# Optimization experiments

Hardware: AMD Instinct MI355X
Metric: run time of the kernel (lower is better)

The kernel has to match this reference:

```python
import jax, jax.numpy as jnp
import numpy as np

IN_DIM = 256
QK_DIM = IN_DIM // 8


def setup_inputs() -> dict:
    key = jax.random.key(0)
    ks = jax.random.split(key, 10)
    B, C, W, H = 4, IN_DIM, 64, 64
    a = jax.random.normal(ks[0], (B, C, W, H), dtype=jnp.float32)
    b = jax.random.normal(ks[1], (B, C, W, H), dtype=jnp.float32)
    c = jax.random.uniform(ks[2], (B, 1, 2 * W, 2 * H), dtype=jnp.float32)
    scale = 0.02
    wq = jax.random.normal(ks[3], (QK_DIM, C), dtype=jnp.float32) * scale
    bq = jnp.zeros((QK_DIM,), dtype=jnp.float32)
    wk = jax.random.normal(ks[4], (QK_DIM, C), dtype=jnp.float32) * scale
    bk = jnp.zeros((QK_DIM,), dtype=jnp.float32)
    wv = jax.random.normal(ks[5], (C, C), dtype=jnp.float32) * scale
    bv = jnp.zeros((C,), dtype=jnp.float32)
    gamma = jnp.ones((1,), dtype=jnp.float32)
    return {"a": a, "b": b, "c": c, "wq": wq, "bq": bq, "wk": wk,
            "bk": bk, "wv": wv, "bv": bv, "gamma": gamma}


def reference(a, b, c, wq, bq, wk, bk, wv, bv, gamma):
    B, C, W, H = a.shape
    N = W * H
    # F.interpolate(c, scale_factor=1/down_rate, mode='nearest'): output idx i -> input idx i*down_rate
    down = c.shape[2] // W
    cd = c[:, :, ::down, ::down]                      # [B,1,W,H]
    # 1x1 convs as channel contractions
    q = jnp.einsum('bchw,oc->bohw', a, wq) + bq[None, :, None, None]
    k = jnp.einsum('bchw,oc->bohw', b, wk) + bk[None, :, None, None]
    v = jnp.einsum('bchw,oc->bohw', a, wv) + bv[None, :, None, None]
    qf = q.reshape(B, QK_DIM, N)                      # proj_query^T rows are spatial
    kf = k.reshape(B, QK_DIM, N)
    vf = v.reshape(B, C, N)
    sim = jnp.einsum('bdi,bdj->bij', qf, kf)          # [B,N,N]
    cflat = cd.reshape(B, N)
    # mask[b,i,j] = cflat[b,i] (per-query multiplicative logit scaling)
    logits = sim * cflat[:, :, None]
    attn = jax.nn.softmax(logits, axis=-1)            # [B,N,N]
    out_attn = jnp.einsum('bcj,bij->bci', vf, attn).reshape(B, C, W, H)
    out = gamma * a * cd + (1.0 - cd) * out_attn
    return out
```

## Files before the change

### kernel.cpp

```cpp
#include <hip/hip_runtime.h>

#define LOG2E 1.44269504088896340736f

typedef __attribute__((ext_vector_type(8))) short short8;
typedef __attribute__((ext_vector_type(4))) float float4v;
typedef __attribute__((ext_vector_type(2))) float float2v;
typedef __attribute__((ext_vector_type(2))) int int2v;
typedef __attribute__((ext_vector_type(4))) int int4v;

__device__ inline unsigned short f2bf(float f) {
    union { float f; unsigned u; } v; v.f = f;
    unsigned r = v.u + 0x7fffu + ((v.u >> 16) & 1u);
    return (unsigned short)(r >> 16);
}
__device__ inline float bf2f(unsigned short u) {
    union { unsigned u; float f; } v; v.u = ((unsigned)u) << 16;
    return v.f;
}
__device__ inline unsigned pk_bf16(float a, float b) {
    union { float f; unsigned u; } ua, ub; ua.f = a; ub.f = b;
    return __builtin_amdgcn_perm(ub.u + 0x8000u, ua.u + 0x8000u, 0x07060302u);
}
__device__ inline unsigned cvtpk_bf16(float a, float b) {
    unsigned r;
    asm("v_cvt_pk_bf16_f32 %0, %1, %2" : "=v"(r) : "v"(a), "v"(b));
    return r;
}

__global__ void wcvt_kernel(const float* __restrict__ wq, const float* __restrict__ wk,
                            const float* __restrict__ wv, unsigned short* __restrict__ Wbf)
{
    int idx = blockIdx.x * 256 + threadIdx.x;
    int e4  = idx * 4;
    int row = e4 >> 8, col = e4 & 255;
    const float* src = (row < 32) ? (wq + row * 256 + col)
                     : (row < 64) ? (wk + (row - 32) * 256 + col)
                                  : (wv + (row - 64) * 256 + col);
    float4v v = *(const float4v*)src;
    int2v p;
    p.x = (unsigned)f2bf(v[0]) | ((unsigned)f2bf(v[1]) << 16);
    p.y = (unsigned)f2bf(v[2]) | ((unsigned)f2bf(v[3]) << 16);
    *(int2v*)(Wbf + e4) = p;
}

__launch_bounds__(512, 4)
__global__ void proj_kernel(const float* __restrict__ a_p, const float* __restrict__ b_p,
                            const float* __restrict__ c_p,
                            const float* __restrict__ bq, const float* __restrict__ bk,
                            const float* __restrict__ bv,
                            const unsigned short* __restrict__ Wbf,
                            unsigned short* __restrict__ Qg, unsigned short* __restrict__ Kg,
                            unsigned short* __restrict__ Vg)
{
    __shared__ __align__(16) unsigned short At[32 * 266];
    __shared__ __align__(16) unsigned short Bt[32 * 266];
    __shared__ float bias[320];
    __shared__ float cdl[32];

    const int t    = threadIdx.x;
    const int blk  = blockIdx.x;
    const int b    = blk & 3;
    const int tile = blk >> 2;
    const int i0   = tile * 32;
    const int lane = t & 63;
    const int w    = t >> 6;
    const int q    = lane >> 4;
    const int n    = lane & 15;
    const int it   = w & 1;
    const int mh   = w >> 1;

    {
        const int arr = t >> 8, tt = t & 255;
        unsigned* dst = (unsigned*)(arr ? Bt : At);
        const float* base = (arr ? b_p : a_p) + (size_t)b * 256 * 4096 + i0;
#pragma unroll
        for (int r = 0; r < 4; ++r) {
            int task = r * 256 + tt;
            int cp = task >> 3, px4 = (task & 7) * 4;
            const float* s0 = base + (size_t)(2 * cp) * 4096 + px4;
            float4v r0 = *(const float4v*)s0;
            float4v r1 = *(const float4v*)(s0 + 4096);
#pragma unroll
            for (int k = 0; k < 4; ++k)
                dst[(px4 + k) * 133 + cp] = pk_bf16(r0[k], r1[k]);
        }
        if (t < 320) bias[t] = (t < 32) ? bq[t] : (t < 64) ? bk[t - 32] : bv[t - 64];
        else if (t < 352) {
            int u = t - 320;
            cdl[u] = c_p[b * 16384 + (tile >> 1) * 256 + (tile & 1) * 64 + u * 2];
        }
    }
    __syncthreads();

    float4v acc[5];
#pragma unroll
    for (int j = 0; j < 5; ++j) acc[j] = (float4v){0.f, 0.f, 0.f, 0.f};

#pragma unroll 2
    for (int kc = 0; kc < 8; ++kc) {
        short8 xa = *(const short8*)&At[(it * 16 + n) * 266 + kc * 32 + q * 8];
        short8 xb = xa;
        if (mh == 0)
            xb = *(const short8*)&Bt[(it * 16 + n) * 266 + kc * 32 + q * 8];
#pragma unroll
        for (int j = 0; j < 5; ++j) {
            int mt = mh * 5 + j;
            short8 wf = *(const short8*)(Wbf + (size_t)(mt * 16 + n) * 256 + kc * 32 + q * 8);
            short8 bsel = (mt == 2 || mt == 3) ? xb : xa;
            acc[j] = __builtin_amdgcn_mfma_f32_16x16x32_bf16(wf, bsel, acc[j], 0, 0, 0);
        }
    }
    __syncthreads();

    unsigned short* QKst = At;
    unsigned short* Vst  = Bt;
    {
        const float cdq = cdl[it * 16 + n] * LOG2E;
#pragma unroll
        for (int j = 0; j < 5; ++j) {
            int mt = mh * 5 + j;
            float4v bv4 = *(const float4v*)&bias[mt * 16 + q * 4];
            float v0 = acc[j][0] + bv4[0], v1 = acc[j][1] + bv4[1];
            float v2 = acc[j][2] + bv4[2], v3 = acc[j][3] + bv4[3];
            if (mt < 2) {
                v0 *= cdq; v1 *= cdq; v2 *= cdq; v3 *= cdq;
                int2v pk; pk.x = (int)pk_bf16(v0, v1); pk.y = (int)pk_bf16(v2, v3);
                *(int2v*)&QKst[(it * 16 + n) * 72 + mt * 16 + q * 4] = pk;
            } else if (mt < 4) {
                int2v pk; pk.x = (int)pk_bf16(v0, v1); pk.y = (int)pk_bf16(v2, v3);
                *(int2v*)&QKst[(it * 16 + n) * 72 + mt * 16 + q * 4] = pk;
            } else {
                int p = ((n >> 2) * 8) + (it * 4) + (n & 3);
                int cbase = mt * 16 - 64 + q * 4;
                Vst[(cbase + 0) * 32 + p] = f2bf(v0);
                Vst[(cbase + 1) * 32 + p] = f2bf(v1);
                Vst[(cbase + 2) * 32 + p] = f2bf(v2);
                Vst[(cbase + 3) * 32 + p] = f2bf(v3);
            }
        }
    }
    __syncthreads();

    if (t < 256) {
        int i = t >> 3, h8 = t & 7;
        int4v v = *(const int4v*)&QKst[i * 72 + h8 * 8];
        unsigned short* dstp = (h8 < 4)
            ? Qg + (size_t)(b * 4096 + i0 + i) * 32 + h8 * 8
            : Kg + (size_t)(b * 4096 + i0 + i) * 32 + (h8 - 4) * 8;
        *(int4v*)dstp = v;
    }
    {
#pragma unroll
        for (int k = 0; k < 2; ++k) {
            int flat = k * 512 + t;
            int4v v = *(const int4v*)&Vst[flat * 8];
            *(int4v*)(Vg + (size_t)(b * 128 + tile) * 8192 + (size_t)flat * 8) = v;
        }
    }
}

__launch_bounds__(256, 3)
__global__ void attn_kernel(const unsigned short* __restrict__ Qg,
                            const unsigned short* __restrict__ Kg,
                            const unsigned short* __restrict__ Vg,
                            unsigned short* __restrict__ Opart, float* __restrict__ lsum)
{
    const int t    = threadIdx.x;
    const int blk  = blockIdx.x;
    const int b    = blk & 3;
    const int rt   = (blk >> 2) & 63;
    const int s    = blk >> 8;
    const int ni   = (s == 2) ? 32 : 48;
    const int lidx = (s << 8) | (rt << 2) | b;
    const int i0   = rt * 64;
    const int lane = t & 63;
    const int w    = t >> 6;
    const int q    = lane >> 4;
    const int n    = lane & 15;

    short8 qf[4];
#pragma unroll
    for (int ig = 0; ig < 4; ++ig)
        qf[ig] = *(const short8*)(Qg + (size_t)(b * 4096 + i0 + ig * 16 + n) * 32 + q * 8);

    float4v acc[4][4];
#pragma unroll
    for (int ig = 0; ig < 4; ++ig)
#pragma unroll
        for (int ct = 0; ct < 4; ++ct) acc[ig][ct] = (float4v){0.f, 0.f, 0.f, 0.f};
    float lsc[4] = {0.f, 0.f, 0.f, 0.f};

    const float4v m16v = (float4v){-16.f, -16.f, -16.f, -16.f};

    const unsigned short* kb = Kg + (size_t)(b * 4096 + s * 1536 + n) * 32 + q * 8;
    const unsigned short* vb = Vg + ((size_t)((b * 128 + s * 48) * 256 + w * 64 + n)) * 32 + q * 8;

    short8 vf[4];
#pragma unroll
    for (int ct = 0; ct < 4; ++ct)
        vf[ct] = *(const short8*)(vb + ct * 512);
    short8 kf0 = *(const short8*)(kb);
    short8 kf1 = *(const short8*)(kb + 512);

    short8 pfc[4];
    {
        float4v s0[4], s1[4];
#pragma unroll
        for (int ig = 0; ig < 4; ++ig) {
            s0[ig] = __builtin_amdgcn_mfma_f32_16x16x32_bf16(kf0, qf[ig], m16v, 0, 0, 0);
            s1[ig] = __builtin_amdgcn_mfma_f32_16x16x32_bf16(kf1, qf[ig], m16v, 0, 0, 0);
        }
        kf0 = *(const short8*)(kb + 1024);
        kf1 = *(const short8*)(kb + 1536);
#pragma unroll
        for (int ig = 0; ig < 4; ++ig) {
            float p0 = __builtin_amdgcn_exp2f(s0[ig][0]), p1 = __builtin_amdgcn_exp2f(s0[ig][1]);
            float p2 = __builtin_amdgcn_exp2f(s0[ig][2]), p3 = __builtin_amdgcn_exp2f(s0[ig][3]);
            float p4 = __builtin_amdgcn_exp2f(s1[ig][0]), p5 = __builtin_amdgcn_exp2f(s1[ig][1]);
            float p6 = __builtin_amdgcn_exp2f(s1[ig][2]), p7 = __builtin_amdgcn_exp2f(s1[ig][3]);
            lsc[ig] += ((p0 + p1) + (p2 + p3)) + ((p4 + p5) + (p6 + p7));
            union { short8 s8; unsigned u[4]; } pf_;
            pf_.u[0] = cvtpk_bf16(p0, p1);
            pf_.u[1] = cvtpk_bf16(p2, p3);
            pf_.u[2] = cvtpk_bf16(p4, p5);
            pf_.u[3] = cvtpk_bf16(p6, p7);
            pfc[ig] = pf_.s8;
        }
    }
    kb += 2048;
    vb += 8192;

#pragma unroll 1
    for (int it = 0; it < ni - 1; ++it) {
        float4v s0[4], s1[4];
#pragma unroll
        for (int ig = 0; ig < 4; ++ig) {
            s0[ig] = __builtin_amdgcn_mfma_f32_16x16x32_bf16(kf0, qf[ig], m16v, 0, 0, 0);
            s1[ig] = __builtin_amdgcn_mfma_f32_16x16x32_bf16(kf1, qf[ig], m16v, 0, 0, 0);
        }
        kf0 = *(const short8*)(kb);
        kf1 = *(const short8*)(kb + 512);

        __builtin_amdgcn_s_setprio(1);
#pragma unroll
        for (int ig = 0; ig < 4; ++ig)
#pragma unroll
            for (int ct = 0; ct < 4; ++ct)
                acc[ig][ct] = __builtin_amdgcn_mfma_f32_16x16x32_bf16(pfc[ig], vf[ct], acc[ig][ct], 0, 0, 0);
        __builtin_amdgcn_s_setprio(0);

#pragma unroll
        for (int ct = 0; ct < 4; ++ct)
            vf[ct] = *(const short8*)(vb + ct * 512);

#pragma unroll
        for (int ig = 0; ig < 4; ++ig) {
            float p0 = __builtin_amdgcn_exp2f(s0[ig][0]), p1 = __builtin_amdgcn_exp2f(s0[ig][1]);
            float p2 = __builtin_amdgcn_exp2f(s0[ig][2]), p3 = __builtin_amdgcn_exp2f(s0[ig][3]);
            float p4 = __builtin_amdgcn_exp2f(s1[ig][0]), p5 = __builtin_amdgcn_exp2f(s1[ig][1]);
            float p6 = __builtin_amdgcn_exp2f(s1[ig][2]), p7 = __builtin_amdgcn_exp2f(s1[ig][3]);
            lsc[ig] += ((p0 + p1) + (p2 + p3)) + ((p4 + p5) + (p6 + p7));
            union { short8 s8; unsigned u[4]; } pf_;
            pf_.u[0] = cvtpk_bf16(p0, p1);
            pf_.u[1] = cvtpk_bf16(p2, p3);
            pf_.u[2] = cvtpk_bf16(p4, p5);
            pf_.u[3] = cvtpk_bf16(p6, p7);
            pfc[ig] = pf_.s8;
        }

        kb += 1024;
        vb += 8192;
    }

#pragma unroll
    for (int ig = 0; ig < 4; ++ig)
#pragma unroll
        for (int ct = 0; ct < 4; ++ct)
            acc[ig][ct] = __builtin_amdgcn_mfma_f32_16x16x32_bf16(pfc[ig], vf[ct], acc[ig][ct], 0, 0, 0);

    const size_t obase = (size_t)lidx * 16384;
#pragma unroll
    for (int ig = 0; ig < 4; ++ig)
#pragma unroll
        for (int ct = 0; ct < 4; ++ct) {
            int c = w * 64 + ct * 16 + n;
            int i = ig * 16 + q * 4;
            int2v pk;
            pk.x = (int)pk_bf16(acc[ig][ct][0], acc[ig][ct][1]);
            pk.y = (int)pk_bf16(acc[ig][ct][2], acc[ig][ct][3]);
            *(int2v*)(Opart + obase + (size_t)c * 64 + i) = pk;
        }
#pragma unroll
    for (int ig = 0; ig < 4; ++ig) {
        float v = lsc[ig];
        v += __shfl_xor(v, 16, 64);
        v += __shfl_xor(v, 32, 64);
        if (w == 0 && lane < 16)
            lsum[(size_t)lidx * 64 + ig * 16 + lane] = v;
    }
}

__launch_bounds__(256, 4)
__global__ void combine_kernel(const float* __restrict__ a_p, const float* __restrict__ c_p,
                               const float* __restrict__ gamma_p,
                               const unsigned short* __restrict__ Opart,
                               const float* __restrict__ lsum, float* __restrict__ out)
{
    __shared__ float invL[64];
    __shared__ float cdl[64];

    const int t   = threadIdx.x;
    const int blk = blockIdx.x;
    const int b   = blk & 3;
    const int rt  = (blk >> 2) & 63;
    const int cs  = blk >> 8;
    const int i0  = rt * 64;

    if (t < 64) {
        float L = 0.f;
#pragma unroll
        for (int s = 0; s < 3; ++s)
            L += lsum[(size_t)((s << 8) | (rt << 2) | b) * 64 + t];
        invL[t] = 1.0f / L;
        cdl[t] = c_p[b * 16384 + rt * 256 + 2 * t];
    }
    __syncthreads();

    const float gam = gamma_p[0];
    const int c  = cs * 32 + (t >> 3);
    const int e8 = (t & 7) * 8;
    float o[8];
#pragma unroll
    for (int r = 0; r < 8; ++r) o[r] = 0.f;
#pragma unroll
    for (int s = 0; s < 3; ++s) {
        int idx = (s << 8) | (rt << 2) | b;
        int4v pv = *(const int4v*)(Opart + (size_t)idx * 16384 + (size_t)c * 64 + e8);
#pragma unroll
        for (int h = 0; h < 4; ++h) {
            unsigned u = (unsigned)pv[h];
            o[2 * h]     += bf2f((unsigned short)(u & 0xffffu));
            o[2 * h + 1] += bf2f((unsigned short)(u >> 16));
        }
    }
    size_t gi = (size_t)(b * 256 + c) * 4096 + i0 + e8;
    float4v a0 = *(const float4v*)(a_p + gi);
    float4v a1 = *(const float4v*)(a_p + gi + 4);
    float4v ov0, ov1;
#pragma unroll
    for (int r = 0; r < 4; ++r) {
        float cd0 = cdl[e8 + r],     l0 = invL[e8 + r];
        float cd1 = cdl[e8 + 4 + r], l1 = invL[e8 + 4 + r];
        ov0[r] = gam * a0[r] * cd0 + (1.0f - cd0) * (o[r] * l0);
        ov1[r] = gam * a1[r] * cd1 + (1.0f - cd1) * (o[4 + r] * l1);
    }
    *(float4v*)(out + gi) = ov0;
    *(float4v*)(out + gi + 4) = ov1;
}

extern "C" void kernel_launch(void* const* d_in, const int* in_sizes, int n_in,
                              void* d_out, int out_size, void* d_ws, size_t ws_size,
                              hipStream_t stream)
{
    const float* a_p   = (const float*)d_in[0];
    const float* b_p   = (const float*)d_in[1];
    const float* c_p   = (const float*)d_in[2];
    const float* wq    = (const float*)d_in[3];
    const float* bq    = (const float*)d_in[4];
    const float* wk    = (const float*)d_in[5];
    const float* bk    = (const float*)d_in[6];
    const float* wv    = (const float*)d_in[7];
    const float* bv    = (const float*)d_in[8];
    const float* gamma = (const float*)d_in[9];
    float* out = (float*)d_out;

    unsigned short* Qg    = (unsigned short*)d_ws;
    unsigned short* Kg    = Qg + (size_t)4 * 4096 * 32;
    unsigned short* Vg    = Kg + (size_t)4 * 4096 * 32;
    unsigned short* Wbf   = Vg + (size_t)4 * 256 * 4096;
    unsigned short* Opart = Wbf + (size_t)320 * 256;
    float*          lsum  = (float*)(Opart + (size_t)768 * 16384);

    wcvt_kernel<<<80, 256, 0, stream>>>(wq, wk, wv, Wbf);
    proj_kernel<<<512, 512, 0, stream>>>(a_p, b_p, c_p, bq, bk, bv, Wbf, Qg, Kg, Vg);
    attn_kernel<<<768, 256, 0, stream>>>(Qg, Kg, Vg, Opart, lsum);
    combine_kernel<<<2048, 256, 0, stream>>>(a_p, c_p, gamma, Opart, lsum, out);
}
```

Measured before the change: 180.6 us.

## Fuse weight bf16 conversion into projection kernel and double pixel tile

Removes the separate weight-conversion kernel launch. The projection kernel now reads fp32 weights directly and converts them to bf16 on the fly. Each block covers 64 pixels instead of 32, so it launches half as many blocks, and each wave computes 10 output tiles instead of 5. This saves a launch and the Wbf round trip, but every block converts weights redundantly, and the larger tile raises register and LDS use and lowers occupancy.

```diff
diff --git a/kernel.cpp b/kernel.cpp
--- a/kernel.cpp
+++ b/kernel.cpp
@@ -27,56 +27,41 @@
     return r;
 }
 
-__global__ void wcvt_kernel(const float* __restrict__ wq, const float* __restrict__ wk,
-                            const float* __restrict__ wv, unsigned short* __restrict__ Wbf)
-{
-    int idx = blockIdx.x * 256 + threadIdx.x;
-    int e4  = idx * 4;
-    int row = e4 >> 8, col = e4 & 255;
-    const float* src = (row < 32) ? (wq + row * 256 + col)
-                     : (row < 64) ? (wk + (row - 32) * 256 + col)
-                                  : (wv + (row - 64) * 256 + col);
-    float4v v = *(const float4v*)src;
-    int2v p;
-    p.x = (unsigned)f2bf(v[0]) | ((unsigned)f2bf(v[1]) << 16);
-    p.y = (unsigned)f2bf(v[2]) | ((unsigned)f2bf(v[3]) << 16);
-    *(int2v*)(Wbf + e4) = p;
-}
-
-__launch_bounds__(512, 4)
+__launch_bounds__(512, 2)
 __global__ void proj_kernel(const float* __restrict__ a_p, const float* __restrict__ b_p,
                             const float* __restrict__ c_p,
+                            const float* __restrict__ wq_p, const float* __restrict__ wk_p,
+                            const float* __restrict__ wv_p,
                             const float* __restrict__ bq, const float* __restrict__ bk,
                             const float* __restrict__ bv,
-                            const unsigned short* __restrict__ Wbf,
                             unsigned short* __restrict__ Qg, unsigned short* __restrict__ Kg,
                             unsigned short* __restrict__ Vg)
 {
-    __shared__ __align__(16) unsigned short At[32 * 266];
-    __shared__ __align__(16) unsigned short Bt[32 * 266];
+    __shared__ __align__(16) unsigned short At[64 * 266];
+    __shared__ __align__(16) unsigned short Bt[64 * 266];
     __shared__ float bias[320];
-    __shared__ float cdl[32];
+    __shared__ float cdl[64];
 
     const int t    = threadIdx.x;
     const int blk  = blockIdx.x;
     const int b    = blk & 3;
     const int tile = blk >> 2;
-    const int i0   = tile * 32;
+    const int i0   = tile * 64;
     const int lane = t & 63;
     const int w    = t >> 6;
     const int q    = lane >> 4;
     const int n    = lane & 15;
-    const int it   = w & 1;
-    const int mh   = w >> 1;
+    const int it   = w & 3;
+    const int mh   = w >> 2;
 
     {
         const int arr = t >> 8, tt = t & 255;
         unsigned* dst = (unsigned*)(arr ? Bt : At);
         const float* base = (arr ? b_p : a_p) + (size_t)b * 256 * 4096 + i0;
 #pragma unroll
-        for (int r = 0; r < 4; ++r) {
+        for (int r = 0; r < 8; ++r) {
             int task = r * 256 + tt;
-            int cp = task >> 3, px4 = (task & 7) * 4;
+            int cp = task >> 4, px4 = (task & 15) * 4;
             const float* s0 = base + (size_t)(2 * cp) * 4096 + px4;
             float4v r0 = *(const float4v*)s0;
             float4v r1 = *(const float4v*)(s0 + 4096);
@@ -85,16 +70,13 @@
                 dst[(px4 + k) * 133 + cp] = pk_bf16(r0[k], r1[k]);
         }
         if (t < 320) bias[t] = (t < 32) ? bq[t] : (t < 64) ? bk[t - 32] : bv[t - 64];
-        else if (t < 352) {
-            int u = t - 320;
-            cdl[u] = c_p[b * 16384 + (tile >> 1) * 256 + (tile & 1) * 64 + u * 2];
-        }
+        else if (t < 384) cdl[t - 320] = c_p[b * 16384 + tile * 256 + (t - 320) * 2];
     }
     __syncthreads();
 
-    float4v acc[5];
-#pragma unroll
-    for (int j = 0; j < 5; ++j) acc[j] = (float4v){0.f, 0.f, 0.f, 0.f};
+    float4v acc[10];
+#pragma unroll
+    for (int j = 0; j < 10; ++j) acc[j] = (float4v){0.f, 0.f, 0.f, 0.f};
 
 #pragma unroll 2
     for (int kc = 0; kc < 8; ++kc) {
@@ -103,11 +85,21 @@
         if (mh == 0)
             xb = *(const short8*)&Bt[(it * 16 + n) * 266 + kc * 32 + q * 8];
 #pragma unroll
-        for (int j = 0; j < 5; ++j) {
-            int mt = mh * 5 + j;
-            short8 wf = *(const short8*)(Wbf + (size_t)(mt * 16 + n) * 256 + kc * 32 + q * 8);
+        for (int j = 0; j < 10; ++j) {
+            int mt = mh * 10 + j;
+            const float* wbase = (mt < 2) ? wq_p : (mt < 4) ? wk_p : wv_p;
+            int mrow = (mt < 2) ? (mt * 16 + n) : (mt < 4) ? ((mt - 2) * 16 + n)
+                                                           : ((mt - 4) * 16 + n);
+            const float* wp = wbase + (size_t)mrow * 256 + kc * 32 + q * 8;
+            float4v wa = *(const float4v*)wp;
+            float4v wb2 = *(const float4v*)(wp + 4);
+            union { short8 s8; unsigned u[4]; } wf_;
+            wf_.u[0] = pk_bf16(wa[0], wa[1]);
+            wf_.u[1] = pk_bf16(wa[2], wa[3]);
+            wf_.u[2] = pk_bf16(wb2[0], wb2[1]);
+            wf_.u[3] = pk_bf16(wb2[2], wb2[3]);
             short8 bsel = (mt == 2 || mt == 3) ? xb : xa;
-            acc[j] = __builtin_amdgcn_mfma_f32_16x16x32_bf16(wf, bsel, acc[j], 0, 0, 0);
+            acc[j] = __builtin_amdgcn_mfma_f32_16x16x32_bf16(wf_.s8, bsel, acc[j], 0, 0, 0);
         }
     }
     __syncthreads();
@@ -117,8 +109,8 @@
     {
         const float cdq = cdl[it * 16 + n] * LOG2E;
 #pragma unroll
-        for (int j = 0; j < 5; ++j) {
-            int mt = mh * 5 + j;
+        for (int j = 0; j < 10; ++j) {
+            int mt = mh * 10 + j;
             float4v bv4 = *(const float4v*)&bias[mt * 16 + q * 4];
             float v0 = acc[j][0] + bv4[0], v1 = acc[j][1] + bv4[1];
             float v2 = acc[j][2] + bv4[2], v3 = acc[j][3] + bv4[3];
@@ -130,18 +122,19 @@
                 int2v pk; pk.x = (int)pk_bf16(v0, v1); pk.y = (int)pk_bf16(v2, v3);
                 *(int2v*)&QKst[(it * 16 + n) * 72 + mt * 16 + q * 4] = pk;
             } else {
-                int p = ((n >> 2) * 8) + (it * 4) + (n & 3);
+                int p = ((n >> 2) * 8) + ((it & 1) * 4) + (n & 3);
                 int cbase = mt * 16 - 64 + q * 4;
-                Vst[(cbase + 0) * 32 + p] = f2bf(v0);
-                Vst[(cbase + 1) * 32 + p] = f2bf(v1);
-                Vst[(cbase + 2) * 32 + p] = f2bf(v2);
-                Vst[(cbase + 3) * 32 + p] = f2bf(v3);
+                int jb = it >> 1;
+                Vst[((jb * 256) + cbase + 0) * 32 + p] = f2bf(v0);
+                Vst[((jb * 256) + cbase + 1) * 32 + p] = f2bf(v1);
+                Vst[((jb * 256) + cbase + 2) * 32 + p] = f2bf(v2);
+                Vst[((jb * 256) + cbase + 3) * 32 + p] = f2bf(v3);
             }
         }
     }
     __syncthreads();
 
-    if (t < 256) {
+    {
         int i = t >> 3, h8 = t & 7;
         int4v v = *(const int4v*)&QKst[i * 72 + h8 * 8];
         unsigned short* dstp = (h8 < 4)
@@ -151,10 +144,11 @@
     }
     {
 #pragma unroll
-        for (int k = 0; k < 2; ++k) {
+        for (int k = 0; k < 4; ++k) {
             int flat = k * 512 + t;
             int4v v = *(const int4v*)&Vst[flat * 8];
-            *(int4v*)(Vg + (size_t)(b * 128 + tile) * 8192 + (size_t)flat * 8) = v;
+            int jb = flat >> 10;
+            *(int4v*)(Vg + (size_t)(b * 128 + tile * 2 + jb) * 8192 + (flat & 1023) * 8) = v;
         }
     }
 }
@@ -377,12 +371,10 @@
     unsigned short* Qg    = (unsigned short*)d_ws;
     unsigned short* Kg    = Qg + (size_t)4 * 4096 * 32;
     unsigned short* Vg    = Kg + (size_t)4 * 4096 * 32;
-    unsigned short* Wbf   = Vg + (size_t)4 * 256 * 4096;
-    unsigned short* Opart = Wbf + (size_t)320 * 256;
+    unsigned short* Opart = Vg + (size_t)4 * 256 * 4096;
     float*          lsum  = (float*)(Opart + (size_t)768 * 16384);
 
-    wcvt_kernel<<<80, 256, 0, stream>>>(wq, wk, wv, Wbf);
-    proj_kernel<<<512, 512, 0, stream>>>(a_p, b_p, c_p, bq, bk, bv, Wbf, Qg, Kg, Vg);
+    proj_kernel<<<256, 512, 0, stream>>>(a_p, b_p, c_p, wq, wk, wv, bq, bk, bv, Qg, Kg, Vg);
     attn_kernel<<<768, 256, 0, stream>>>(Qg, Kg, Vg, Opart, lsum);
     combine_kernel<<<2048, 256, 0, stream>>>(a_p, c_p, gamma, Opart, lsum, out);
 }
```

Result: slower. 190.8 us (+5.7%).
